# Kernel tuning notes

Hardware: AMD Instinct MI355X
Metric: run time of the kernel (lower is better)

## Reference

```python
import jax, jax.numpy as jnp
import numpy as np

NEG = -1e9


def _lstm_step(x, h, c, W_ih, W_hh, b_ih, b_hh):
    # torch LSTM gate order: i, f, g, o
    gates = x @ W_ih.T + b_ih + h @ W_hh.T + b_hh
    i, f, g, o = jnp.split(gates, 4, axis=-1)
    c_new = jax.nn.sigmoid(f) * c + jax.nn.sigmoid(i) * jnp.tanh(g)
    h_new = jax.nn.sigmoid(o) * jnp.tanh(c_new)
    return h_new, c_new


def _forward(encoder_states, emb, W_ih, W_hh, b_ih, b_hh, W_att,
             pad_mask, pointer_mask, token_ids, target_sequence,
             sos_token, eos_token, output_len):
    B, N, D = encoder_states.shape
    V = emb.shape[0]
    dt = encoder_states.dtype
    padf = pad_mask.astype(dt)
    enc = encoder_states * padf[..., None]          # zero padded node states
    # _init_lstm_state: mean of encoder states over valid nodes (pad-only mask)
    h0 = enc.sum(axis=1) / padf.sum(axis=1, keepdims=True)  # [B, D]
    # attention mask after pointer restriction: only valid leaf pointer nodes
    attn_mask = jnp.where(pointer_mask, jnp.asarray(0.0, dt), jnp.asarray(NEG, dt))
    n_ptr = pointer_mask.sum(axis=1).astype(dt)     # [B]
    thr = 1.0 / n_ptr                               # _threshold_cf = 1.0
    b_idx = jnp.arange(B)

    # teacher forcing: step 1 uses SOS, step s>1 uses target_sequence[s-1]
    sos_row = jnp.full((1, B), sos_token, dtype=target_sequence.dtype)
    inputs = jnp.concatenate([sos_row, target_sequence[1:output_len - 1]], axis=0)  # [T-1, B]

    def step(carry, inp):
        h, c = carry
        x = emb[inp]                                     # [B, E]
        h, c = _lstm_step(x, h, c, W_ih, W_hh, b_ih, b_hh)
        # Luong attention -> probabilities over tree nodes
        scores = jnp.einsum('bnd,bd->bn', enc, h @ W_att.T) + attn_mask
        probs = jax.nn.softmax(scores, axis=1)           # [B, N]
        # threshold: probabilities below 1/n_ptr are zeroed; only pointer nodes kept
        probs = jnp.where(pointer_mask & (probs >= thr[:, None]), probs, jnp.asarray(0.0, dt))
        # scatter(reduce='sum') node probabilities into vocab-sized output
        out = jnp.zeros((B, V), dt).at[b_idx[:, None], token_ids].add(probs)
        out = out.at[:, eos_token].set(1.0 - probs.sum(axis=1))
        return (h, c), out

    (_, _), outs = jax.lax.scan(step, (h0, h0), inputs)   # [T-1, B, V]
    out0 = jnp.zeros((B, V), dt).at[:, sos_token].set(1.0)
    return jnp.concatenate([out0[None], outs], axis=0)    # [T, B, V]


def setup_inputs() -> dict:
    key = jax.random.key(0)
    ks = jax.random.split(key, 10)
    B, N, D, E, V, T = 32, 2048, 512, 512, 32000, 32
    encoder_states = jax.random.normal(ks[0], (B, N, D), dtype=jnp.float32)
    lengths = jax.random.randint(ks[1], (B,), N // 2, N + 1)
    pad_mask = jnp.arange(N)[None, :] < lengths[:, None]            # [B, N] ragged trees
    leaf = jax.random.bernoulli(ks[2], 0.5, (B, N))
    pointer_mask = pad_mask & leaf                                  # valid leaf pointer nodes
    token_ids = jax.random.randint(ks[3], (B, N), 0, V, dtype=jnp.int32)
    target_sequence = jax.random.randint(ks[4], (T, B), 3, V, dtype=jnp.int32)
    s = 0.02
    emb = jax.random.normal(ks[5], (V, E), dtype=jnp.float32) * s
    W_ih = jax.random.normal(ks[6], (4 * D, E), dtype=jnp.float32) * s
    W_hh = jax.random.normal(ks[7], (4 * D, D), dtype=jnp.float32) * s
    b_ih = jnp.zeros((4 * D,), dtype=jnp.float32)
    b_hh = jnp.zeros((4 * D,), dtype=jnp.float32)
    W_att = jax.random.normal(ks[8], (D, D), dtype=jnp.float32) * s
    return {
        'encoder_states': encoder_states, 'emb': emb,
        'W_ih': W_ih, 'W_hh': W_hh, 'b_ih': b_ih, 'b_hh': b_hh, 'W_att': W_att,
        'pad_mask': pad_mask, 'pointer_mask': pointer_mask,
        'token_ids': token_ids, 'target_sequence': target_sequence,
        'sos_token': 1, 'eos_token': 2, 'output_len': T,
    }


def reference(encoder_states, emb, W_ih, W_hh, b_ih, b_hh, W_att,
              pad_mask, pointer_mask, token_ids, target_sequence,
              sos_token, eos_token, output_len):
    return _forward(encoder_states, emb, W_ih, W_hh, b_ih, b_hh, W_att,
                    pad_mask, pointer_mask, token_ids, target_sequence,
                    sos_token, eos_token, output_len)
```

## Files before the change

### kernel.cpp

```cpp
#include <hip/hip_runtime.h>
#include <math.h>

#define BB 32
#define NN 2048
#define DD 512
#define VV 32000
#define NSTEP 31

__device__ inline float sigm(float x){ return 1.0f/(1.0f+expf(-x)); }
__device__ inline float dot4(float4 a, float4 b){
  return a.x*b.x + a.y*b.y + a.z*b.z + a.w*b.w;
}

__device__ inline float red8(float a0,float a1,float a2,float a3,
                             float a4,float a5,float a6,float a7,int lane){
  float m01 = ((lane&1)? a1:a0) + __shfl_xor(((lane&1)? a0:a1),1,64);
  float m23 = ((lane&1)? a3:a2) + __shfl_xor(((lane&1)? a2:a3),1,64);
  float m45 = ((lane&1)? a5:a4) + __shfl_xor(((lane&1)? a4:a5),1,64);
  float m67 = ((lane&1)? a7:a6) + __shfl_xor(((lane&1)? a6:a7),1,64);
  float m03 = ((lane&2)? m23:m01) + __shfl_xor(((lane&2)? m01:m23),2,64);
  float m47 = ((lane&2)? m67:m45) + __shfl_xor(((lane&2)? m45:m67),2,64);
  float m   = ((lane&4)? m47:m03) + __shfl_xor(((lane&4)? m03:m47),4,64);
  m += __shfl_xor(m,8,64); m += __shfl_xor(m,16,64); m += __shfl_xor(m,32,64);
  return m;
}

__global__ __launch_bounds__(256) void k_cnt(
    const int* __restrict__ pad, const int* __restrict__ pmask,
    const int* __restrict__ sosp,
    float* __restrict__ cntp, float* __restrict__ thr, float* __restrict__ out) {
  __shared__ int r1[256], r2[256];
  int b = blockIdx.x, tid = threadIdx.x;
  float4* orow4 = (float4*)(out + (size_t)b*VV);
  float4 z = {0.f,0.f,0.f,0.f};
  for (int i = tid; i < VV/4; i += 256) orow4[i] = z;
  int cp = 0, cq = 0;
  for (int n = tid; n < NN; n += 256) { cp += pad[b*NN+n]; cq += pmask[b*NN+n]; }
  r1[tid] = cp; r2[tid] = cq; __syncthreads();
  for (int st = 128; st; st >>= 1) {
    if (tid < st) { r1[tid] += r1[tid+st]; r2[tid] += r2[tid+st]; }
    __syncthreads();
  }
  if (tid == 0) {
    cntp[b] = (float)r1[0];
    thr[b]  = 1.0f/(float)r2[0];
    out[(size_t)b*VV + sosp[0]] = 1.0f;
  }
}

__global__ __launch_bounds__(128) void k_meanpart(
    const float* __restrict__ enc, const int* __restrict__ pad,
    float* __restrict__ hpart) {
  int b = blockIdx.x, ch = blockIdx.y, kq = threadIdx.x;
  int n0 = ch*32;
  float4 acc = {0.f,0.f,0.f,0.f};
#pragma unroll 8
  for (int r = 0; r < 32; r++) {
    int n = n0 + r;
    float msk = (float)pad[b*NN + n];
    float4 v = *(const float4*)(enc + ((size_t)(b*NN + n))*DD + kq*4);
    acc.x += msk*v.x; acc.y += msk*v.y; acc.z += msk*v.z; acc.w += msk*v.w;
  }
  *(float4*)(hpart + ((size_t)(b*64 + ch))*DD + kq*4) = acc;
}

__global__ __launch_bounds__(128) void k_meanfin(
    const float* __restrict__ hpart, const float* __restrict__ cntp,
    float* __restrict__ h0, float* __restrict__ c) {
  int b = blockIdx.x, kq = threadIdx.x;
  float4 acc = {0.f,0.f,0.f,0.f};
  for (int ch = 0; ch < 64; ch++) {
    float4 v = *(const float4*)(hpart + ((size_t)(b*64 + ch))*DD + kq*4);
    acc.x += v.x; acc.y += v.y; acc.z += v.z; acc.w += v.w;
  }
  float ic = 1.0f/cntp[b];
  acc.x *= ic; acc.y *= ic; acc.z *= ic; acc.w *= ic;
  *(float4*)(h0 + b*DD + kq*4) = acc;
  *(float4*)(c  + b*DD + kq*4) = acc;
}

__global__ __launch_bounds__(256) void k_g0(
    const float* __restrict__ emb, const float* __restrict__ Wih,
    const float* __restrict__ bih, const float* __restrict__ bhh,
    const int* __restrict__ target, const int* __restrict__ sosp,
    float* __restrict__ G0) {
  int nt = blockIdx.x, mg = blockIdx.y;
  int w = threadIdx.x>>6, lane = threadIdx.x&63;
  int m0 = mg*32 + w*8;
  float4 x0[8], x1[8];
#pragma unroll
  for (int j = 0; j < 8; j++) {
    int m = m0 + j, s = m >> 5, bb = m & 31;
    int tok = (s == 0) ? sosp[0] : target[s*BB + bb];
    const float* xp = emb + (size_t)tok*DD + lane*4;
    x0[j] = *(const float4*)xp;
    x1[j] = *(const float4*)(xp + 256);
  }
  int r0 = nt*32;
#pragma unroll 2
  for (int i = 0; i < 32; i++) {
    int r = r0 + i;
    const float* wp = Wih + (size_t)r*DD + lane*4;
    float4 w0 = *(const float4*)wp, w1 = *(const float4*)(wp + 256);
    float a0 = dot4(w0,x0[0]) + dot4(w1,x1[0]);
    float a1 = dot4(w0,x0[1]) + dot4(w1,x1[1]);
    float a2 = dot4(w0,x0[2]) + dot4(w1,x1[2]);
    float a3 = dot4(w0,x0[3]) + dot4(w1,x1[3]);
    float a4 = dot4(w0,x0[4]) + dot4(w1,x1[4]);
    float a5 = dot4(w0,x0[5]) + dot4(w1,x1[5]);
    float a6 = dot4(w0,x0[6]) + dot4(w1,x1[6]);
    float a7 = dot4(w0,x0[7]) + dot4(w1,x1[7]);
    float v = red8(a0,a1,a2,a3,a4,a5,a6,a7,lane) + bih[r] + bhh[r];
    if (lane < 8) G0[(size_t)(m0 + lane)*2048 + r] = v;
  }
}

__global__ __launch_bounds__(512) void k_hstep(
    const float* __restrict__ hin, const float* __restrict__ Whh,
    const float* __restrict__ G0s, float* __restrict__ c,
    float* __restrict__ hout) {
  __shared__ float g[BB*8];
  int bi = blockIdx.x, d0 = bi*2;
  int tid = threadIdx.x;
  int w = tid>>6, lane = tid&63;
  float4 W0[8], W1[8];
#pragma unroll
  for (int j = 0; j < 8; j++) {
    int r = (j>>1)*DD + d0 + (j&1);
    const float* wp = Whh + (size_t)r*DD + lane*4;
    W0[j] = *(const float4*)wp; W1[j] = *(const float4*)(wp + 256);
  }
#pragma unroll
  for (int bb = 0; bb < 4; bb++) {
    int b = w*4 + bb;
    const float* hp = hin + b*DD + lane*4;
    float4 h0v = *(const float4*)hp, h1v = *(const float4*)(hp + 256);
    float a0 = dot4(h0v,W0[0]) + dot4(h1v,W1[0]);
    float a1 = dot4(h0v,W0[1]) + dot4(h1v,W1[1]);
    float a2 = dot4(h0v,W0[2]) + dot4(h1v,W1[2]);
    float a3 = dot4(h0v,W0[3]) + dot4(h1v,W1[3]);
    float a4 = dot4(h0v,W0[4]) + dot4(h1v,W1[4]);
    float a5 = dot4(h0v,W0[5]) + dot4(h1v,W1[5]);
    float a6 = dot4(h0v,W0[6]) + dot4(h1v,W1[6]);
    float a7 = dot4(h0v,W0[7]) + dot4(h1v,W1[7]);
    float v = red8(a0,a1,a2,a3,a4,a5,a6,a7,lane);
    if (lane < 8) g[b*8 + lane] = v;
  }
  __syncthreads();
  if (tid < 64) {
    int b = tid>>1, dd = tid&1;
    const float* G = G0s + (size_t)b*2048 + d0 + dd;
    float gi = g[b*8 + 0 + dd] + G[0];
    float gf = g[b*8 + 2 + dd] + G[512];
    float gg = g[b*8 + 4 + dd] + G[1024];
    float go = g[b*8 + 6 + dd] + G[1536];
    int ci = b*DD + d0 + dd;
    float cn = sigm(gf)*c[ci] + sigm(gi)*tanhf(gg);
    float hn = sigm(go)*tanhf(cn);
    c[ci] = cn; hout[ci] = hn;
  }
}

__global__ __launch_bounds__(256) void k_qallw(
    const float* __restrict__ H, const float* __restrict__ Watt,
    float* __restrict__ Q) {
  int nt = blockIdx.x, mg = blockIdx.y;
  int w = threadIdx.x>>6, lane = threadIdx.x&63;
  int m0 = mg*32 + w*8;
  float4 x0[8], x1[8];
#pragma unroll
  for (int j = 0; j < 8; j++) {
    const float* xp = H + (size_t)(m0 + j)*DD + lane*4;
    x0[j] = *(const float4*)xp; x1[j] = *(const float4*)(xp + 256);
  }
  int r0 = nt*16;
#pragma unroll 2
  for (int i = 0; i < 16; i++) {
    int r = r0 + i;
    const float* wp = Watt + (size_t)r*DD + lane*4;
    float4 w0 = *(const float4*)wp, w1 = *(const float4*)(wp + 256);
    float a0 = dot4(w0,x0[0]) + dot4(w1,x1[0]);
    float a1 = dot4(w0,x0[1]) + dot4(w1,x1[1]);
    float a2 = dot4(w0,x0[2]) + dot4(w1,x1[2]);
    float a3 = dot4(w0,x0[3]) + dot4(w1,x1[3]);
    float a4 = dot4(w0,x0[4]) + dot4(w1,x1[4]);
    float a5 = dot4(w0,x0[5]) + dot4(w1,x1[5]);
    float a6 = dot4(w0,x0[6]) + dot4(w1,x1[6]);
    float a7 = dot4(w0,x0[7]) + dot4(w1,x1[7]);
    float v = red8(a0,a1,a2,a3,a4,a5,a6,a7,lane);
    if (lane < 8) Q[(size_t)(m0 + lane)*DD + r] = v;
  }
}

__global__ __launch_bounds__(256) void k_scores3(
    const float* __restrict__ enc, const float* __restrict__ Q,
    float* __restrict__ S) {
  int nt = blockIdx.x, b = blockIdx.y;
  int w = threadIdx.x>>6, lane = threadIdx.x&63;
  int s0 = w*8;
  float4 q0[8], q1[8];
#pragma unroll
  for (int j = 0; j < 8; j++) {
    const float* qp = Q + (size_t)((s0 + j)*BB + b)*DD + lane*4;
    q0[j] = *(const float4*)qp; q1[j] = *(const float4*)(qp + 256);
  }
  int n0 = nt*32;
  int sl = s0 + (lane & 7);
#pragma unroll 2
  for (int i = 0; i < 32; i++) {
    int n = n0 + i;
    const float* ep = enc + ((size_t)(b*NN + n))*DD + lane*4;
    float4 e0 = *(const float4*)ep, e1 = *(const float4*)(ep + 256);
    float a0 = dot4(e0,q0[0]) + dot4(e1,q1[0]);
    float a1 = dot4(e0,q0[1]) + dot4(e1,q1[1]);
    float a2 = dot4(e0,q0[2]) + dot4(e1,q1[2]);
    float a3 = dot4(e0,q0[3]) + dot4(e1,q1[3]);
    float a4 = dot4(e0,q0[4]) + dot4(e1,q1[4]);
    float a5 = dot4(e0,q0[5]) + dot4(e1,q1[5]);
    float a6 = dot4(e0,q0[6]) + dot4(e1,q1[6]);
    float a7 = dot4(e0,q0[7]) + dot4(e1,q1[7]);
    float v = red8(a0,a1,a2,a3,a4,a5,a6,a7,lane);
    if (lane < 8 && sl < NSTEP) S[((size_t)sl*BB + b)*NN + n] = v;
  }
}

__global__ __launch_bounds__(256) void k_scatter2(
    const float* __restrict__ S, const int* __restrict__ pmask,
    const int* __restrict__ tok, const float* __restrict__ thr,
    const int* __restrict__ eosp, float* __restrict__ out) {
  __shared__ float red[256];
  __shared__ float ex[NN];
  int s = blockIdx.x, b = blockIdx.y, tid = threadIdx.x;
  float* orow = out + ((size_t)(s+1)*BB + b)*VV;
  float4 z = {0.f,0.f,0.f,0.f};
  float4* orow4 = (float4*)orow;
  for (int i = tid; i < VV/4; i += 256) orow4[i] = z;
  const float* sr = S + ((size_t)s*BB + b)*NN;
  const int* pm = pmask + b*NN;
  float m = -3.4e38f;
  for (int n = tid; n < NN; n += 256) if (pm[n]) m = fmaxf(m, sr[n]);
  red[tid] = m; __syncthreads();
  for (int st = 128; st; st >>= 1) {
    if (tid < st) red[tid] = fmaxf(red[tid], red[tid+st]);
    __syncthreads();
  }
  float smax = red[0]; __syncthreads();
  float sum = 0.f;
  for (int n = tid; n < NN; n += 256) {
    float e = pm[n] ? expf(sr[n] - smax) : 0.f;
    ex[n] = e; sum += e;
  }
  red[tid] = sum; __syncthreads();
  for (int st = 128; st; st >>= 1) {
    if (tid < st) red[tid] += red[tid+st];
    __syncthreads();
  }
  float inv = 1.0f/red[0];
  float th = thr[b];
  float keep = 0.f;
  for (int n = tid; n < NN; n += 256) {
    float p = ex[n]*inv;
    if (p >= th) { atomicAdd(orow + tok[b*NN + n], p); keep += p; }
  }
  __syncthreads();
  red[tid] = keep; __syncthreads();
  for (int st = 128; st; st >>= 1) {
    if (tid < st) red[tid] += red[tid+st];
    __syncthreads();
  }
  if (tid == 0) orow[eosp[0]] = 1.0f - red[0];
}

extern "C" void kernel_launch(void* const* d_in, const int* in_sizes, int n_in,
                              void* d_out, int out_size, void* d_ws, size_t ws_size,
                              hipStream_t stream) {
  const float* enc   = (const float*)d_in[0];
  const float* emb   = (const float*)d_in[1];
  const float* Wih   = (const float*)d_in[2];
  const float* Whh   = (const float*)d_in[3];
  const float* bih   = (const float*)d_in[4];
  const float* bhh   = (const float*)d_in[5];
  const float* Watt  = (const float*)d_in[6];
  const int*   pad   = (const int*)d_in[7];
  const int*   pmask = (const int*)d_in[8];
  const int*   tok   = (const int*)d_in[9];
  const int*   target= (const int*)d_in[10];
  const int*   sosp  = (const int*)d_in[11];
  const int*   eosp  = (const int*)d_in[12];
  float* out = (float*)d_out;

  float* w    = (float*)d_ws;
  float* c    = w;
  float* h0   = c    + BB*DD;
  float* H    = h0   + BB*DD;
  float* Q    = H    + NSTEP*BB*DD;
  float* S    = Q    + 32*BB*DD;
  float* G0   = S    + (size_t)NSTEP*BB*NN;
  float* cntp = G0   + (size_t)992*2048;
  float* thr  = cntp + 32;
  float* hpart = G0;

  k_cnt<<<32, 256, 0, stream>>>(pad, pmask, sosp, cntp, thr, out);
  k_meanpart<<<dim3(32,64), 128, 0, stream>>>(enc, pad, hpart);
  k_meanfin<<<32, 128, 0, stream>>>(hpart, cntp, h0, c);

  k_g0<<<dim3(64,31), 256, 0, stream>>>(emb, Wih, bih, bhh, target, sosp, G0);

  for (int s = 0; s < NSTEP; s++) {
    const float* hin = (s == 0) ? h0 : (H + (size_t)(s-1)*BB*DD);
    k_hstep<<<256, 512, 0, stream>>>(hin, Whh, G0 + (size_t)s*BB*2048, c,
                                     H + (size_t)s*BB*DD);
  }

  k_qallw<<<dim3(32,31), 256, 0, stream>>>(H, Watt, Q);
  k_scores3<<<dim3(64,32), 256, 0, stream>>>(enc, Q, S);
  k_scatter2<<<dim3(NSTEP,32), 256, 0, stream>>>(S, pmask, tok, thr, eosp, out);
}
```

Measured before the change: 663.1 us.

## Fuse per-step LSTM kernels into one persistent cooperative kernel with grid sync

Replaces 31 separate k_hstep launches with one cooperative kernel that loops over the time steps and uses grid.sync between them. W_hh stays in registers across steps, and the cell state is kept in a register instead of being read and written in global memory. This removes per-launch overhead and repeated weight loads. The cost is a grid-wide barrier per step, and the launch depends on all 256 blocks of 512 threads being co-resident.

New measurement: 2.590 ms. +290.5%, slower.

```diff
diff --git a/kernel.cpp b/kernel.cpp
--- a/kernel.cpp
+++ b/kernel.cpp
@@ -1,5 +1,8 @@
 #include <hip/hip_runtime.h>
+#include <hip/hip_cooperative_groups.h>
 #include <math.h>
+
+namespace cg = cooperative_groups;
 
 #define BB 32
 #define NN 2048
@@ -115,10 +118,10 @@
   }
 }
 
-__global__ __launch_bounds__(512) void k_hstep(
-    const float* __restrict__ hin, const float* __restrict__ Whh,
-    const float* __restrict__ G0s, float* __restrict__ c,
-    float* __restrict__ hout) {
+__global__ __launch_bounds__(512) void k_hloop(
+    const float* __restrict__ h0, const float* __restrict__ Whh,
+    const float* __restrict__ G0, float* __restrict__ H) {
+  cg::grid_group grid = cg::this_grid();
   __shared__ float g[BB*8];
   int bi = blockIdx.x, d0 = bi*2;
   int tid = threadIdx.x;
@@ -130,34 +133,45 @@
     const float* wp = Whh + (size_t)r*DD + lane*4;
     W0[j] = *(const float4*)wp; W1[j] = *(const float4*)(wp + 256);
   }
-#pragma unroll
-  for (int bb = 0; bb < 4; bb++) {
-    int b = w*4 + bb;
-    const float* hp = hin + b*DD + lane*4;
-    float4 h0v = *(const float4*)hp, h1v = *(const float4*)(hp + 256);
-    float a0 = dot4(h0v,W0[0]) + dot4(h1v,W1[0]);
-    float a1 = dot4(h0v,W0[1]) + dot4(h1v,W1[1]);
-    float a2 = dot4(h0v,W0[2]) + dot4(h1v,W1[2]);
-    float a3 = dot4(h0v,W0[3]) + dot4(h1v,W1[3]);
-    float a4 = dot4(h0v,W0[4]) + dot4(h1v,W1[4]);
-    float a5 = dot4(h0v,W0[5]) + dot4(h1v,W1[5]);
-    float a6 = dot4(h0v,W0[6]) + dot4(h1v,W1[6]);
-    float a7 = dot4(h0v,W0[7]) + dot4(h1v,W1[7]);
-    float v = red8(a0,a1,a2,a3,a4,a5,a6,a7,lane);
-    if (lane < 8) g[b*8 + lane] = v;
-  }
-  __syncthreads();
-  if (tid < 64) {
-    int b = tid>>1, dd = tid&1;
-    const float* G = G0s + (size_t)b*2048 + d0 + dd;
-    float gi = g[b*8 + 0 + dd] + G[0];
-    float gf = g[b*8 + 2 + dd] + G[512];
-    float gg = g[b*8 + 4 + dd] + G[1024];
-    float go = g[b*8 + 6 + dd] + G[1536];
-    int ci = b*DD + d0 + dd;
-    float cn = sigm(gf)*c[ci] + sigm(gi)*tanhf(gg);
-    float hn = sigm(go)*tanhf(cn);
-    c[ci] = cn; hout[ci] = hn;
+  int pb = tid>>1, pdd = tid&1;
+  float creg = 0.f;
+  if (tid < 64) creg = h0[pb*DD + d0 + pdd];
+
+  for (int s = 0; s < NSTEP; s++) {
+    const float* hin = (s == 0) ? h0 : (H + (size_t)(s-1)*BB*DD);
+    float Gi = 0.f, Gf = 0.f, Gg = 0.f, Go = 0.f;
+    if (tid < 64) {
+      const float* G = G0 + ((size_t)s*BB + pb)*2048 + d0 + pdd;
+      Gi = G[0]; Gf = G[512]; Gg = G[1024]; Go = G[1536];
+    }
+#pragma unroll
+    for (int bb = 0; bb < 4; bb++) {
+      int b = w*4 + bb;
+      const float* hp = hin + b*DD + lane*4;
+      float4 h0v = *(const float4*)hp, h1v = *(const float4*)(hp + 256);
+      float a0 = dot4(h0v,W0[0]) + dot4(h1v,W1[0]);
+      float a1 = dot4(h0v,W0[1]) + dot4(h1v,W1[1]);
+      float a2 = dot4(h0v,W0[2]) + dot4(h1v,W1[2]);
+      float a3 = dot4(h0v,W0[3]) + dot4(h1v,W1[3]);
+      float a4 = dot4(h0v,W0[4]) + dot4(h1v,W1[4]);
+      float a5 = dot4(h0v,W0[5]) + dot4(h1v,W1[5]);
+      float a6 = dot4(h0v,W0[6]) + dot4(h1v,W1[6]);
+      float a7 = dot4(h0v,W0[7]) + dot4(h1v,W1[7]);
+      float v = red8(a0,a1,a2,a3,a4,a5,a6,a7,lane);
+      if (lane < 8) g[b*8 + lane] = v;
+    }
+    __syncthreads();
+    if (tid < 64) {
+      float gi = g[pb*8 + 0 + pdd] + Gi;
+      float gf = g[pb*8 + 2 + pdd] + Gf;
+      float gg = g[pb*8 + 4 + pdd] + Gg;
+      float go = g[pb*8 + 6 + pdd] + Go;
+      creg = sigm(gf)*creg + sigm(gi)*tanhf(gg);
+      float hn = sigm(go)*tanhf(creg);
+      H[(size_t)s*BB*DD + pb*DD + d0 + pdd] = hn;
+    }
+    __threadfence();
+    grid.sync();
   }
 }
 
@@ -306,10 +320,11 @@
 
   k_g0<<<dim3(64,31), 256, 0, stream>>>(emb, Wih, bih, bhh, target, sosp, G0);
 
-  for (int s = 0; s < NSTEP; s++) {
-    const float* hin = (s == 0) ? h0 : (H + (size_t)(s-1)*BB*DD);
-    k_hstep<<<256, 512, 0, stream>>>(hin, Whh, G0 + (size_t)s*BB*2048, c,
-                                     H + (size_t)s*BB*DD);
+  {
+    const float* h0c = h0;
+    void* hargs[] = { (void*)&h0c, (void*)&Whh, (void*)&G0, (void*)&H };
+    hipLaunchCooperativeKernel((const void*)k_hloop, dim3(256), dim3(512),
+                               hargs, 0, stream);
   }
 
   k_qallw<<<dim3(32,31), 256, 0, stream>>>(H, Watt, Q);
```
